# Kernel optimization log

Hardware: AMD Instinct MI355X
Metric: run time of the kernel (lower is better)

Reference implementation:

```python
import jax, jax.numpy as jnp
import numpy as np

HIDDEN = 512
INPUT = 128
SEQ = 512
BATCH = 128
ALPHA = 0.5          # dt / tau = 1 / 2
NOISE_STD = 0.05


def setup_inputs() -> dict:
    key = jax.random.key(0)
    k_x, k_wi, k_wh, k_n = jax.random.split(key, 4)
    inp = jax.random.normal(k_x, (SEQ, BATCH, INPUT), dtype=jnp.float32)
    # input layer: uniform dist (as in LinearLayer default 'uniform'), no bias
    lim = 1.0 / np.sqrt(INPUT)
    W_in = jax.random.uniform(k_wi, (HIDDEN, INPUT), minval=-lim, maxval=lim, dtype=jnp.float32)
    # hidden layer: normal dist, scaled ~ 1/sqrt(N) for unit spectral radius
    W_hid = jax.random.normal(k_wh, (HIDDEN, HIDDEN), dtype=jnp.float32) / np.sqrt(HIDDEN)
    # per-step noise, shared across batch, pre-scaled by std
    noise = jax.random.normal(k_n, (SEQ, HIDDEN), dtype=jnp.float32) * NOISE_STD
    return {"input": inp, "W_in": W_in, "W_hid": W_hid, "noise": noise}


def reference(input, W_in, W_hid, noise):
    # pre-compute the input projection for all steps: (S, B, H)
    proj_in = jnp.einsum('sbi,hi->sbh', input, W_in)

    def step(h, xs):
        x_t, n_t = xs                      # (B,H), (H,)
        hidden_out = jnp.einsum('bh,gh->bg', jax.nn.relu(h), W_hid)
        h_new = (1.0 - ALPHA) * h + ALPHA * (hidden_out + x_t + n_t)
        return h_new, h_new

    h0 = jnp.zeros((input.shape[1], HIDDEN), dtype=input.dtype)
    hidden, output = jax.lax.scan(step, h0, (proj_in, noise))
    return output, hidden
```

## Files before the change

### kernel.cpp

```cpp
#include <hip/hip_runtime.h>
#include <hip/hip_bf16.h>


#define SEQ   512
#define NB    128
#define NI    128
#define NH    512
#define WBG   8
#define WGG   16
#define BT    16
#define GT    32

typedef __attribute__((ext_vector_type(8))) short  short8;
typedef __attribute__((ext_vector_type(4))) float  float4v;
typedef __attribute__((ext_vector_type(4))) int    int4v;
typedef __attribute__((ext_vector_type(2))) int    int2v;

static __device__ __forceinline__ unsigned short f2bf(float f) {
    __hip_bfloat16 h = __float2bfloat16(f);
    unsigned short u;
    __builtin_memcpy(&u, &h, 2);
    return u;
}

static __device__ __forceinline__ short8 pack8(float4v a, float4v b) {
    short8 r;
    r[0] = (short)f2bf(a[0]); r[1] = (short)f2bf(a[1]);
    r[2] = (short)f2bf(a[2]); r[3] = (short)f2bf(a[3]);
    r[4] = (short)f2bf(b[0]); r[5] = (short)f2bf(b[1]);
    r[6] = (short)f2bf(b[2]); r[7] = (short)f2bf(b[3]);
    return r;
}

#define LOADR(idx, off) \
    asm volatile("global_load_dwordx4 %0, %1, off offset:" #off " sc0 sc1" \
                 : "=v"(rv[idx]) : "v"(rbase));

__global__ __launch_bounds__(64, 1) void rnn_step_kernel(
    const float* __restrict__ xin,
    const float* __restrict__ w_in,
    const float* __restrict__ w_hid,
    const float* __restrict__ noise,
    float*       __restrict__ out,
    unsigned short*            xbuf)
{
    const int lane = threadIdx.x;
    const int r16  = lane & 15;
    const int kg   = lane >> 4;
    const int ib   = blockIdx.x & 7;
    const int jg   = blockIdx.x >> 3;
    const int b0   = ib * BT;
    const int g0   = jg * GT;

    short8 wf[2][16];
#pragma unroll
    for (int t = 0; t < 2; ++t)
#pragma unroll
        for (int c = 0; c < 16; ++c) {
            const float* p = w_hid + (size_t)(g0 + t * 16 + r16) * NH + c * 32 + kg * 8;
            wf[t][c] = pack8(*(const float4v*)p, *(const float4v*)(p + 4));
        }
    short8 wfin[2][4];
#pragma unroll
    for (int t = 0; t < 2; ++t)
#pragma unroll
        for (int c = 0; c < 4; ++c) {
            const float* p = w_in + (size_t)(g0 + t * 16 + r16) * NI + c * 32 + kg * 8;
            wfin[t][c] = pack8(*(const float4v*)p, *(const float4v*)(p + 4));
        }

    float4v h0 = {0.f, 0.f, 0.f, 0.f};
    float4v h1 = {0.f, 0.f, 0.f, 0.f};

    const float* inp  = xin + (size_t)(b0 + r16) * NI + kg * 8;
    const float* nzp  = noise + g0 + kg * 4;
    float*       outp = out + (size_t)(b0 + r16) * NH + g0 + kg * 4;

    const unsigned long long xbase  = (unsigned long long)(uintptr_t)xbuf;
    const unsigned long long xw_off = ((unsigned long long)(b0 + r16) * NH + g0 + kg * 4) * 2ull;
    const unsigned long long xr_off = ((unsigned long long)(b0 + r16) * NH + kg * 8) * 2ull;
    const unsigned long long bufstride = (unsigned long long)NB * NH * 2ull;

#pragma unroll 1
    for (int s = 0; s < SEQ; ++s) {
        const float* ip = inp + (size_t)s * NB * NI;
        short8 bin[4];
#pragma unroll
        for (int c = 0; c < 4; ++c) {
            float4v a = *(const float4v*)(ip + c * 32);
            float4v b = *(const float4v*)(ip + c * 32 + 4);
            bin[c] = pack8(a, b);
        }
        const float* np_ = nzp + (size_t)s * NH;
        float4v nz0 = *(const float4v*)np_;
        float4v nz1 = *(const float4v*)(np_ + 16);

        float4v acc0 = {0.f, 0.f, 0.f, 0.f};
        float4v acc1 = {0.f, 0.f, 0.f, 0.f};
#pragma unroll
        for (int c = 0; c < 4; ++c) {
            acc0 = __builtin_amdgcn_mfma_f32_16x16x32_bf16(wfin[0][c], bin[c], acc0, 0, 0, 0);
            acc1 = __builtin_amdgcn_mfma_f32_16x16x32_bf16(wfin[1][c], bin[c], acc1, 0, 0, 0);
        }

        if (s > 0) {
            const unsigned expTag = ((unsigned)(s - 1) >> 1) & 1u;
            unsigned long long rbase = xbase + (unsigned long long)((s - 1) & 1) * bufstride + xr_off;
            int4v rv[16];
            unsigned guard = 0;
            for (;;) {
                LOADR(0, 0)    LOADR(1, 64)   LOADR(2, 128)  LOADR(3, 192)
                LOADR(4, 256)  LOADR(5, 320)  LOADR(6, 384)  LOADR(7, 448)
                LOADR(8, 512)  LOADR(9, 576)  LOADR(10, 640) LOADR(11, 704)
                LOADR(12, 768) LOADR(13, 832) LOADR(14, 896) LOADR(15, 960)
                asm volatile("s_waitcnt vmcnt(0)"
                             : "+v"(rv[0]), "+v"(rv[1]), "+v"(rv[2]), "+v"(rv[3]),
                               "+v"(rv[4]), "+v"(rv[5]), "+v"(rv[6]), "+v"(rv[7]),
                               "+v"(rv[8]), "+v"(rv[9]), "+v"(rv[10]), "+v"(rv[11]),
                               "+v"(rv[12]), "+v"(rv[13]), "+v"(rv[14]), "+v"(rv[15])
                             :
                             : "memory");
                bool ok;
                if (expTag) {
                    unsigned a = 0xFFFFFFFFu;
#pragma unroll
                    for (int c = 0; c < 16; ++c)
                        a &= (unsigned)(rv[c][0] & rv[c][1] & rv[c][2] & rv[c][3]);
                    ok = (a & 0x80008000u) == 0x80008000u;
                } else {
                    unsigned o = 0u;
#pragma unroll
                    for (int c = 0; c < 16; ++c)
                        o |= (unsigned)(rv[c][0] | rv[c][1] | rv[c][2] | rv[c][3]);
                    ok = (o & 0x80008000u) == 0u;
                }
                if (__all(ok) || ++guard >= (1u << 16)) break;
            }
            __builtin_amdgcn_sched_barrier(0);

            if (expTag) {
#pragma unroll
                for (int c = 0; c < 16; ++c) {
                    rv[c][0] &= 0x7FFF7FFF; rv[c][1] &= 0x7FFF7FFF;
                    rv[c][2] &= 0x7FFF7FFF; rv[c][3] &= 0x7FFF7FFF;
                }
            }

            float4v p0a = {0.f,0.f,0.f,0.f}, p0b = {0.f,0.f,0.f,0.f};
            float4v p1a = {0.f,0.f,0.f,0.f}, p1b = {0.f,0.f,0.f,0.f};
#pragma unroll
            for (int c = 0; c < 8; ++c) {
                short8 rb0 = __builtin_bit_cast(short8, rv[c]);
                short8 rb1 = __builtin_bit_cast(short8, rv[c + 8]);
                p0a = __builtin_amdgcn_mfma_f32_16x16x32_bf16(wf[0][c],     rb0, p0a, 0, 0, 0);
                p0b = __builtin_amdgcn_mfma_f32_16x16x32_bf16(wf[0][c + 8], rb1, p0b, 0, 0, 0);
                p1a = __builtin_amdgcn_mfma_f32_16x16x32_bf16(wf[1][c],     rb0, p1a, 0, 0, 0);
                p1b = __builtin_amdgcn_mfma_f32_16x16x32_bf16(wf[1][c + 8], rb1, p1b, 0, 0, 0);
            }
#pragma unroll
            for (int r = 0; r < 4; ++r) {
                acc0[r] += p0a[r] + p0b[r];
                acc1[r] += p1a[r] + p1b[r];
            }
        }

        float4v hn0, hn1;
#pragma unroll
        for (int r = 0; r < 4; ++r) {
            hn0[r] = 0.5f * h0[r] + 0.5f * (acc0[r] + nz0[r]);
            hn1[r] = 0.5f * h1[r] + 0.5f * (acc1[r] + nz1[r]);
        }
        h0 = hn0; h1 = hn1;

        const unsigned tmask = ((s >> 1) & 1) ? 0x80008000u : 0u;
        unsigned q0 = ((unsigned)f2bf(fmaxf(hn0[0], 0.f)) | ((unsigned)f2bf(fmaxf(hn0[1], 0.f)) << 16)) | tmask;
        unsigned q1 = ((unsigned)f2bf(fmaxf(hn0[2], 0.f)) | ((unsigned)f2bf(fmaxf(hn0[3], 0.f)) << 16)) | tmask;
        unsigned q2 = ((unsigned)f2bf(fmaxf(hn1[0], 0.f)) | ((unsigned)f2bf(fmaxf(hn1[1], 0.f)) << 16)) | tmask;
        unsigned q3 = ((unsigned)f2bf(fmaxf(hn1[2], 0.f)) | ((unsigned)f2bf(fmaxf(hn1[3], 0.f)) << 16)) | tmask;
        int2v e0; e0[0] = (int)q0; e0[1] = (int)q1;
        int2v e1; e1[0] = (int)q2; e1[1] = (int)q3;
        unsigned long long wb = xbase + (unsigned long long)(s & 1) * bufstride + xw_off;
        asm volatile("s_waitcnt vmcnt(0)" ::: "memory");
        asm volatile("global_store_dwordx2 %0, %1, off sc0 sc1" :: "v"(wb), "v"(e0) : "memory");
        asm volatile("global_store_dwordx2 %0, %1, off offset:32 sc0 sc1" :: "v"(wb), "v"(e1) : "memory");

        float* op = outp + (size_t)s * NB * NH;
        *(float4v*)op        = hn0;
        *(float4v*)(op + 16) = hn1;
        if (s == SEQ - 1) {
            float* tp = out + (size_t)SEQ * NB * NH + (size_t)(b0 + r16) * NH + g0 + kg * 4;
            *(float4v*)tp        = hn0;
            *(float4v*)(tp + 16) = hn1;
        }
    }
}

extern "C" void kernel_launch(void* const* d_in, const int* in_sizes, int n_in,
                              void* d_out, int out_size, void* d_ws, size_t ws_size,
                              hipStream_t stream) {
    (void)in_sizes; (void)n_in; (void)out_size; (void)ws_size;
    const float* xin   = (const float*)d_in[0];
    const float* w_in  = (const float*)d_in[1];
    const float* w_hid = (const float*)d_in[2];
    const float* noise = (const float*)d_in[3];
    float* out = (float*)d_out;

    unsigned short* xbuf = (unsigned short*)d_ws;

    hipMemsetAsync(d_ws, 0xAA, 2 * NB * NH * sizeof(unsigned short), stream);
    hipLaunchKernelGGL(rnn_step_kernel, dim3(WBG * WGG), dim3(64), 0, stream,
                       xin, w_in, w_hid, noise, out, xbuf);
}
```

Measured before the change: 1.471 ms.

## Split input projection into separate kernel and share hidden state via LDS across waves

The input projection moves out of the recurrent loop into a separate parallel MFMA kernel that writes into the output buffer, which the scan kernel then reads back with prefetch. The scan now uses 16 workgroups of 8 waves. Each pair of workgroups covers one batch chain and half the hidden units each, and the per-step hidden state is exchanged through a swizzled LDS buffer with barriers. Global flag-polling shrinks from 16 loads per wave to one small load of the peer half, which cuts the cross-CU traffic on the per-step critical path. The cost is a block barrier each step and reliance on a peer workgroup being co-resident.

```diff
diff --git a/kernel.cpp b/kernel.cpp
--- a/kernel.cpp
+++ b/kernel.cpp
@@ -2,19 +2,17 @@
 #include <hip/hip_bf16.h>
 
 
-#define SEQ   512
-#define NB    128
-#define NI    128
-#define NH    512
-#define WBG   8
-#define WGG   16
-#define BT    16
-#define GT    32
+#define SEQ 512
+#define NB  128
+#define NI  128
+#define NH  512
 
 typedef __attribute__((ext_vector_type(8))) short  short8;
 typedef __attribute__((ext_vector_type(4))) float  float4v;
 typedef __attribute__((ext_vector_type(4))) int    int4v;
 typedef __attribute__((ext_vector_type(2))) int    int2v;
+
+#define SWZ(b, cb) ((cb) ^ (((b) & 7) << 4))
 
 static __device__ __forceinline__ unsigned short f2bf(float f) {
     __hip_bfloat16 h = __float2bfloat16(f);
@@ -32,159 +30,202 @@
     return r;
 }
 
-#define LOADR(idx, off) \
-    asm volatile("global_load_dwordx4 %0, %1, off offset:" #off " sc0 sc1" \
-                 : "=v"(rv[idx]) : "v"(rbase));
-
-__global__ __launch_bounds__(64, 1) void rnn_step_kernel(
+#define BARLDS() do { \
+    asm volatile("s_waitcnt lgkmcnt(0)" ::: "memory"); \
+    asm volatile("s_barrier" ::: "memory"); } while (0)
+
+__global__ __launch_bounds__(256) void proj_kernel(
     const float* __restrict__ xin,
     const float* __restrict__ w_in,
+    float*       __restrict__ out)
+{
+    const int lane = threadIdx.x & 63;
+    const int wv   = threadIdx.x >> 6;
+    const int r16  = lane & 15;
+    const int kg   = lane >> 4;
+    const int rt   = blockIdx.x;
+    const int g0   = blockIdx.y * 128 + wv * 32;
+
+    short8 wfin[2][4];
+#pragma unroll
+    for (int t = 0; t < 2; ++t)
+#pragma unroll
+        for (int c = 0; c < 4; ++c) {
+            const float* p = w_in + (size_t)(g0 + t * 16 + r16) * NI + c * 32 + kg * 8;
+            wfin[t][c] = pack8(*(const float4v*)p, *(const float4v*)(p + 4));
+        }
+    const float* xp = xin + (size_t)(rt * 16 + r16) * NI + kg * 8;
+    short8 bin[4];
+#pragma unroll
+    for (int c = 0; c < 4; ++c)
+        bin[c] = pack8(*(const float4v*)(xp + c * 32), *(const float4v*)(xp + c * 32 + 4));
+
+    float4v a0 = {0.f, 0.f, 0.f, 0.f};
+    float4v a1 = {0.f, 0.f, 0.f, 0.f};
+#pragma unroll
+    for (int c = 0; c < 4; ++c) {
+        a0 = __builtin_amdgcn_mfma_f32_16x16x32_bf16(wfin[0][c], bin[c], a0, 0, 0, 0);
+        a1 = __builtin_amdgcn_mfma_f32_16x16x32_bf16(wfin[1][c], bin[c], a1, 0, 0, 0);
+    }
+    float* op = out + (size_t)(rt * 16 + r16) * NH + g0 + kg * 4;
+    *(float4v*)op        = a0;
+    *(float4v*)(op + 16) = a1;
+}
+
+__global__ __launch_bounds__(512, 2) void scan_kernel(
     const float* __restrict__ w_hid,
     const float* __restrict__ noise,
     float*       __restrict__ out,
-    unsigned short*            xbuf)
+    unsigned short* __restrict__ gbuf)
 {
-    const int lane = threadIdx.x;
-    const int r16  = lane & 15;
-    const int kg   = lane >> 4;
-    const int ib   = blockIdx.x & 7;
-    const int jg   = blockIdx.x >> 3;
-    const int b0   = ib * BT;
-    const int g0   = jg * GT;
-
-    short8 wf[2][16];
+    __shared__ char lds_raw[32768];
+    char* lds = lds_raw;
+
+    const int lane  = threadIdx.x & 63;
+    const int wv    = threadIdx.x >> 6;
+    const int r16   = lane & 15;
+    const int kg    = lane >> 4;
+    const int chain = blockIdx.x & 7;
+    const int H     = blockIdx.x >> 3;
+    const int b0    = chain * 16;
+    const int g0    = H * 256 + wv * 32;
+    const int cLoc  = H * 8;
+    const int cRem  = (1 - H) * 8;
+
+    short8 wfL[2][8], wfR[2][8];
 #pragma unroll
     for (int t = 0; t < 2; ++t)
 #pragma unroll
-        for (int c = 0; c < 16; ++c) {
-            const float* p = w_hid + (size_t)(g0 + t * 16 + r16) * NH + c * 32 + kg * 8;
-            wf[t][c] = pack8(*(const float4v*)p, *(const float4v*)(p + 4));
-        }
-    short8 wfin[2][4];
-#pragma unroll
-    for (int t = 0; t < 2; ++t)
-#pragma unroll
-        for (int c = 0; c < 4; ++c) {
-            const float* p = w_in + (size_t)(g0 + t * 16 + r16) * NI + c * 32 + kg * 8;
-            wfin[t][c] = pack8(*(const float4v*)p, *(const float4v*)(p + 4));
+        for (int j = 0; j < 8; ++j) {
+            const float* pL = w_hid + (size_t)(g0 + t * 16 + r16) * NH + (cLoc + j) * 32 + kg * 8;
+            const float* pR = w_hid + (size_t)(g0 + t * 16 + r16) * NH + (cRem + j) * 32 + kg * 8;
+            wfL[t][j] = pack8(*(const float4v*)pL, *(const float4v*)(pL + 4));
+            wfR[t][j] = pack8(*(const float4v*)pR, *(const float4v*)(pR + 4));
         }
 
     float4v h0 = {0.f, 0.f, 0.f, 0.f};
     float4v h1 = {0.f, 0.f, 0.f, 0.f};
 
-    const float* inp  = xin + (size_t)(b0 + r16) * NI + kg * 8;
-    const float* nzp  = noise + g0 + kg * 4;
-    float*       outp = out + (size_t)(b0 + r16) * NH + g0 + kg * 4;
-
-    const unsigned long long xbase  = (unsigned long long)(uintptr_t)xbuf;
-    const unsigned long long xw_off = ((unsigned long long)(b0 + r16) * NH + g0 + kg * 4) * 2ull;
-    const unsigned long long xr_off = ((unsigned long long)(b0 + r16) * NH + kg * 8) * 2ull;
-    const unsigned long long bufstride = (unsigned long long)NB * NH * 2ull;
+    const float* nzbase = noise + g0 + kg * 4;
+    float*       outrow = out + (size_t)(b0 + r16) * NH + g0 + kg * 4;
+
+    float4v pfp0 = *(const float4v*)outrow;
+    float4v pfp1 = *(const float4v*)(outrow + 16);
+    float4v pfn0 = *(const float4v*)nzbase;
+    float4v pfn1 = *(const float4v*)(nzbase + 16);
+
+    const unsigned long long gb = (unsigned long long)(uintptr_t)gbuf;
+    const unsigned long long myoff =
+        (unsigned long long)(chain * 2 + H) * 8192ull + (unsigned)(r16 * 512 + wv * 64 + kg * 8);
+    const unsigned long long peoff =
+        (unsigned long long)(chain * 2 + (1 - H)) * 8192ull + (unsigned)(r16 * 512 + wv * 64 + kg * 16);
+    const int rdrow = r16 * 1024;
 
 #pragma unroll 1
     for (int s = 0; s < SEQ; ++s) {
-        const float* ip = inp + (size_t)s * NB * NI;
-        short8 bin[4];
-#pragma unroll
-        for (int c = 0; c < 4; ++c) {
-            float4v a = *(const float4v*)(ip + c * 32);
-            float4v b = *(const float4v*)(ip + c * 32 + 4);
-            bin[c] = pack8(a, b);
-        }
-        const float* np_ = nzp + (size_t)s * NH;
-        float4v nz0 = *(const float4v*)np_;
-        float4v nz1 = *(const float4v*)(np_ + 16);
-
-        float4v acc0 = {0.f, 0.f, 0.f, 0.f};
-        float4v acc1 = {0.f, 0.f, 0.f, 0.f};
-#pragma unroll
-        for (int c = 0; c < 4; ++c) {
-            acc0 = __builtin_amdgcn_mfma_f32_16x16x32_bf16(wfin[0][c], bin[c], acc0, 0, 0, 0);
-            acc1 = __builtin_amdgcn_mfma_f32_16x16x32_bf16(wfin[1][c], bin[c], acc1, 0, 0, 0);
+        const float4v prj0 = pfp0, prj1 = pfp1, nz0 = pfn0, nz1 = pfn1;
+        float4v p0a = {0.f,0.f,0.f,0.f}, p0b = {0.f,0.f,0.f,0.f};
+        float4v p1a = {0.f,0.f,0.f,0.f}, p1b = {0.f,0.f,0.f,0.f};
+        const int pb = (s - 1) & 1;
+
+        if (s > 0) {
+            int4v rb[8];
+#pragma unroll
+            for (int j = 0; j < 8; ++j)
+                rb[j] = *(const int4v*)(lds + pb * 16384 + rdrow +
+                                        SWZ(r16, (cLoc + j) * 64 + kg * 16));
+#pragma unroll
+            for (int j = 0; j < 4; ++j) {
+                short8 v = __builtin_bit_cast(short8, rb[j]);
+                p0a = __builtin_amdgcn_mfma_f32_16x16x32_bf16(wfL[0][j], v, p0a, 0, 0, 0);
+                p1a = __builtin_amdgcn_mfma_f32_16x16x32_bf16(wfL[1][j], v, p1a, 0, 0, 0);
+            }
+#pragma unroll
+            for (int j = 4; j < 8; ++j) {
+                short8 v = __builtin_bit_cast(short8, rb[j]);
+                p0b = __builtin_amdgcn_mfma_f32_16x16x32_bf16(wfL[0][j], v, p0b, 0, 0, 0);
+                p1b = __builtin_amdgcn_mfma_f32_16x16x32_bf16(wfL[1][j], v, p1b, 0, 0, 0);
+            }
+        }
+
+        if (s < SEQ - 1) {
+            const float* orow = outrow + (size_t)(s + 1) * NB * NH;
+            pfp0 = *(const float4v*)orow;
+            pfp1 = *(const float4v*)(orow + 16);
+            const float* nrow = nzbase + (size_t)(s + 1) * NH;
+            pfn0 = *(const float4v*)nrow;
+            pfn1 = *(const float4v*)(nrow + 16);
         }
 
         if (s > 0) {
             const unsigned expTag = ((unsigned)(s - 1) >> 1) & 1u;
-            unsigned long long rbase = xbase + (unsigned long long)((s - 1) & 1) * bufstride + xr_off;
-            int4v rv[16];
+            const unsigned long long pa = gb + (unsigned long long)pb * 131072ull + peoff;
+            int4v rv;
             unsigned guard = 0;
             for (;;) {
-                LOADR(0, 0)    LOADR(1, 64)   LOADR(2, 128)  LOADR(3, 192)
-                LOADR(4, 256)  LOADR(5, 320)  LOADR(6, 384)  LOADR(7, 448)
-                LOADR(8, 512)  LOADR(9, 576)  LOADR(10, 640) LOADR(11, 704)
-                LOADR(12, 768) LOADR(13, 832) LOADR(14, 896) LOADR(15, 960)
-                asm volatile("s_waitcnt vmcnt(0)"
-                             : "+v"(rv[0]), "+v"(rv[1]), "+v"(rv[2]), "+v"(rv[3]),
-                               "+v"(rv[4]), "+v"(rv[5]), "+v"(rv[6]), "+v"(rv[7]),
-                               "+v"(rv[8]), "+v"(rv[9]), "+v"(rv[10]), "+v"(rv[11]),
-                               "+v"(rv[12]), "+v"(rv[13]), "+v"(rv[14]), "+v"(rv[15])
-                             :
-                             : "memory");
+                asm volatile("global_load_dwordx4 %0, %1, off sc0 sc1" : "=v"(rv) : "v"(pa));
+                asm volatile("s_waitcnt vmcnt(0)" : "+v"(rv) :: "memory");
                 bool ok;
-                if (expTag) {
-                    unsigned a = 0xFFFFFFFFu;
-#pragma unroll
-                    for (int c = 0; c < 16; ++c)
-                        a &= (unsigned)(rv[c][0] & rv[c][1] & rv[c][2] & rv[c][3]);
-                    ok = (a & 0x80008000u) == 0x80008000u;
-                } else {
-                    unsigned o = 0u;
-#pragma unroll
-                    for (int c = 0; c < 16; ++c)
-                        o |= (unsigned)(rv[c][0] | rv[c][1] | rv[c][2] | rv[c][3]);
-                    ok = (o & 0x80008000u) == 0u;
-                }
-                if (__all(ok) || ++guard >= (1u << 16)) break;
+                if (expTag)
+                    ok = ((unsigned)(rv[0] & rv[1] & rv[2] & rv[3]) & 0x80008000u) == 0x80008000u;
+                else
+                    ok = ((unsigned)(rv[0] | rv[1] | rv[2] | rv[3]) & 0x80008000u) == 0u;
+                if (__all(ok) || ++guard >= (1u << 14)) break;
             }
             __builtin_amdgcn_sched_barrier(0);
-
             if (expTag) {
-#pragma unroll
-                for (int c = 0; c < 16; ++c) {
-                    rv[c][0] &= 0x7FFF7FFF; rv[c][1] &= 0x7FFF7FFF;
-                    rv[c][2] &= 0x7FFF7FFF; rv[c][3] &= 0x7FFF7FFF;
-                }
-            }
-
-            float4v p0a = {0.f,0.f,0.f,0.f}, p0b = {0.f,0.f,0.f,0.f};
-            float4v p1a = {0.f,0.f,0.f,0.f}, p1b = {0.f,0.f,0.f,0.f};
-#pragma unroll
-            for (int c = 0; c < 8; ++c) {
-                short8 rb0 = __builtin_bit_cast(short8, rv[c]);
-                short8 rb1 = __builtin_bit_cast(short8, rv[c + 8]);
-                p0a = __builtin_amdgcn_mfma_f32_16x16x32_bf16(wf[0][c],     rb0, p0a, 0, 0, 0);
-                p0b = __builtin_amdgcn_mfma_f32_16x16x32_bf16(wf[0][c + 8], rb1, p0b, 0, 0, 0);
-                p1a = __builtin_amdgcn_mfma_f32_16x16x32_bf16(wf[1][c],     rb0, p1a, 0, 0, 0);
-                p1b = __builtin_amdgcn_mfma_f32_16x16x32_bf16(wf[1][c + 8], rb1, p1b, 0, 0, 0);
-            }
-#pragma unroll
-            for (int r = 0; r < 4; ++r) {
-                acc0[r] += p0a[r] + p0b[r];
-                acc1[r] += p1a[r] + p1b[r];
+                rv[0] &= 0x7FFF7FFF; rv[1] &= 0x7FFF7FFF;
+                rv[2] &= 0x7FFF7FFF; rv[3] &= 0x7FFF7FFF;
+            }
+            *(int4v*)(lds + pb * 16384 + rdrow + SWZ(r16, (cRem + wv) * 64 + kg * 16)) = rv;
+            BARLDS();
+
+            int4v rr[8];
+#pragma unroll
+            for (int j = 0; j < 8; ++j)
+                rr[j] = *(const int4v*)(lds + pb * 16384 + rdrow +
+                                        SWZ(r16, (cRem + j) * 64 + kg * 16));
+#pragma unroll
+            for (int j = 0; j < 4; ++j) {
+                short8 v = __builtin_bit_cast(short8, rr[j]);
+                p0a = __builtin_amdgcn_mfma_f32_16x16x32_bf16(wfR[0][j], v, p0a, 0, 0, 0);
+                p1a = __builtin_amdgcn_mfma_f32_16x16x32_bf16(wfR[1][j], v, p1a, 0, 0, 0);
+            }
+#pragma unroll
+            for (int j = 4; j < 8; ++j) {
+                short8 v = __builtin_bit_cast(short8, rr[j]);
+                p0b = __builtin_amdgcn_mfma_f32_16x16x32_bf16(wfR[0][j], v, p0b, 0, 0, 0);
+                p1b = __builtin_amdgcn_mfma_f32_16x16x32_bf16(wfR[1][j], v, p1b, 0, 0, 0);
             }
         }
 
         float4v hn0, hn1;
 #pragma unroll
         for (int r = 0; r < 4; ++r) {
-            hn0[r] = 0.5f * h0[r] + 0.5f * (acc0[r] + nz0[r]);
-            hn1[r] = 0.5f * h1[r] + 0.5f * (acc1[r] + nz1[r]);
+            hn0[r] = 0.5f * h0[r] + 0.5f * (p0a[r] + p0b[r] + prj0[r] + nz0[r]);
+            hn1[r] = 0.5f * h1[r] + 0.5f * (p1a[r] + p1b[r] + prj1[r] + nz1[r]);
         }
         h0 = hn0; h1 = hn1;
 
-        const unsigned tmask = ((s >> 1) & 1) ? 0x80008000u : 0u;
-        unsigned q0 = ((unsigned)f2bf(fmaxf(hn0[0], 0.f)) | ((unsigned)f2bf(fmaxf(hn0[1], 0.f)) << 16)) | tmask;
-        unsigned q1 = ((unsigned)f2bf(fmaxf(hn0[2], 0.f)) | ((unsigned)f2bf(fmaxf(hn0[3], 0.f)) << 16)) | tmask;
-        unsigned q2 = ((unsigned)f2bf(fmaxf(hn1[0], 0.f)) | ((unsigned)f2bf(fmaxf(hn1[1], 0.f)) << 16)) | tmask;
-        unsigned q3 = ((unsigned)f2bf(fmaxf(hn1[2], 0.f)) | ((unsigned)f2bf(fmaxf(hn1[3], 0.f)) << 16)) | tmask;
-        int2v e0; e0[0] = (int)q0; e0[1] = (int)q1;
-        int2v e1; e1[0] = (int)q2; e1[1] = (int)q3;
-        unsigned long long wb = xbase + (unsigned long long)(s & 1) * bufstride + xw_off;
-        asm volatile("s_waitcnt vmcnt(0)" ::: "memory");
+        unsigned u0 = (unsigned)f2bf(fmaxf(hn0[0], 0.f)) | ((unsigned)f2bf(fmaxf(hn0[1], 0.f)) << 16);
+        unsigned u1 = (unsigned)f2bf(fmaxf(hn0[2], 0.f)) | ((unsigned)f2bf(fmaxf(hn0[3], 0.f)) << 16);
+        unsigned u2 = (unsigned)f2bf(fmaxf(hn1[0], 0.f)) | ((unsigned)f2bf(fmaxf(hn1[1], 0.f)) << 16);
+        unsigned u3 = (unsigned)f2bf(fmaxf(hn1[2], 0.f)) | ((unsigned)f2bf(fmaxf(hn1[3], 0.f)) << 16);
+        const unsigned tm = ((s >> 1) & 1) ? 0x80008000u : 0u;
+        int2v e0; e0[0] = (int)(u0 | tm); e0[1] = (int)(u1 | tm);
+        int2v e1; e1[0] = (int)(u2 | tm); e1[1] = (int)(u3 | tm);
+        const unsigned long long wb = gb + (unsigned long long)(s & 1) * 131072ull + myoff;
         asm volatile("global_store_dwordx2 %0, %1, off sc0 sc1" :: "v"(wb), "v"(e0) : "memory");
         asm volatile("global_store_dwordx2 %0, %1, off offset:32 sc0 sc1" :: "v"(wb), "v"(e1) : "memory");
 
-        float* op = outp + (size_t)s * NB * NH;
+        int2v l0; l0[0] = (int)u0; l0[1] = (int)u1;
+        int2v l1; l1[0] = (int)u2; l1[1] = (int)u3;
+        const int cb0 = H * 512 + wv * 64 + kg * 8;
+        *(int2v*)(lds + (s & 1) * 16384 + rdrow + SWZ(r16, cb0))      = l0;
+        *(int2v*)(lds + (s & 1) * 16384 + rdrow + SWZ(r16, cb0 + 32)) = l1;
+        BARLDS();
+
+        float* op = outrow + (size_t)s * NB * NH;
         *(float4v*)op        = hn0;
         *(float4v*)(op + 16) = hn1;
         if (s == SEQ - 1) {
@@ -205,9 +246,11 @@
     const float* noise = (const float*)d_in[3];
     float* out = (float*)d_out;
 
-    unsigned short* xbuf = (unsigned short*)d_ws;
-
-    hipMemsetAsync(d_ws, 0xAA, 2 * NB * NH * sizeof(unsigned short), stream);
-    hipLaunchKernelGGL(rnn_step_kernel, dim3(WBG * WGG), dim3(64), 0, stream,
-                       xin, w_in, w_hid, noise, out, xbuf);
-}
+    unsigned short* gbuf = (unsigned short*)d_ws;
+
+    hipMemsetAsync(d_ws, 0xAA, 2 * 16 * 8192, stream);
+    hipLaunchKernelGGL(proj_kernel, dim3(SEQ * NB / 16, 4), dim3(256), 0, stream,
+                       xin, w_in, out);
+    hipLaunchKernelGGL(scan_kernel, dim3(16), dim3(512), 0, stream,
+                       w_hid, noise, out, gbuf);
+}
```

Result: slower. 1.570 ms (+6.7%).
